# Optimization experiments

Hardware: AMD Instinct MI355X
Metric: run time of the kernel (lower is better)

The kernel has to match this reference:

```python
import jax, jax.numpy as jnp
import numpy as np

N, NOBJ, M, H, W = 512, 16, 8192, 128, 128


def _rand_rotations(key, n):
    A = jax.random.normal(key, (n, 3, 3), dtype=jnp.float32)
    q, r = jnp.linalg.qr(A)
    q = q * jnp.sign(jnp.diagonal(r, axis1=-2, axis2=-1))[:, None, :]
    det = jnp.linalg.det(q)  # +-1; flip first column if det == -1
    q = q.at[:, :, 0].multiply(det[:, None])
    return q


def setup_inputs() -> dict:
    key = jax.random.key(0)
    ks = jax.random.split(key, 10)
    obj_id = jax.random.randint(ks[0], (N,), 0, NOBJ, dtype=jnp.int32)
    # realistic pinhole intrinsics (pixels), slight per-sample jitter
    base_K = jnp.array([[600.0, 0.0, 64.0], [0.0, 600.0, 64.0], [0.0, 0.0, 1.0]], jnp.float32)
    cam_K = base_K[None] + jax.random.normal(ks[1], (N, 3, 3)) * jnp.array(
        [[5.0, 0.0, 1.0], [0.0, 5.0, 1.0], [0.0, 0.0, 0.0]], jnp.float32)
    gt_R = _rand_rotations(ks[2], N)
    # small rotational perturbation for pred
    pred_R = _rand_rotations(ks[3], N) @ gt_R
    gt_t = jnp.concatenate([jax.random.normal(ks[4], (N, 2)) * 20.0,
                            500.0 + jax.random.uniform(ks[4], (N, 1)) * 300.0], axis=-1)
    pred_t = gt_t + jax.random.normal(ks[5], (N, 3)) * 5.0
    mesh_points = jax.random.normal(ks[6], (NOBJ, M, 3)) * 50.0  # mm-scale meshes
    diameters = 150.0 + jax.random.uniform(ks[7], (NOBJ,)) * 150.0
    gt_coord_3d_roi = jax.random.normal(ks[8], (N, 3, H, W)) * 50.0
    gt_mask_vis_roi = jax.random.bernoulli(ks[9], 0.4, (N, 1, H, W))
    return dict(obj_id=obj_id, cam_K=cam_K, gt_cam_R_m2c=gt_R, gt_cam_t_m2c=gt_t,
                pred_cam_R_m2c=pred_R, pred_cam_t_m2c=pred_t,
                gt_coord_3d_roi=gt_coord_3d_roi, gt_mask_vis_roi=gt_mask_vis_roi,
                mesh_points=mesh_points, diameters=diameters)


def _project(K, x):
    # K: [N,3,3], x: [N,...,3] -> pixel coords [N,...,2]
    h = jnp.einsum('nij,n...j->n...i', K, x)
    return h[..., :2] / h[..., 2:3]


def reference(obj_id, cam_K, gt_cam_R_m2c, gt_cam_t_m2c, pred_cam_R_m2c,
              pred_cam_t_m2c, gt_coord_3d_roi, gt_mask_vis_roi, mesh_points, diameters):
    # RE (degrees)
    R_diff = pred_cam_R_m2c @ jnp.swapaxes(gt_cam_R_m2c, -2, -1)
    trace = R_diff[..., 0, 0] + R_diff[..., 1, 1] + R_diff[..., 2, 2]
    re = jnp.arccos((jnp.clip(trace, -1.0, 3.0) - 1.0) * 0.5) * (180.0 / jnp.pi)
    # TE (cm)
    te = jnp.linalg.norm(pred_cam_t_m2c - gt_cam_t_m2c, axis=-1) * 100.0
    # ADD: mean distance between transformed mesh points, / diameter
    pts = mesh_points[obj_id]                      # [N,M,3]
    dR = pred_cam_R_m2c - gt_cam_R_m2c
    dt = pred_cam_t_m2c - gt_cam_t_m2c
    diff = jnp.einsum('nij,nmj->nmi', dR, pts) + dt[:, None, :]
    ad = jnp.linalg.norm(diff, axis=-1).mean(axis=-1) / diameters[obj_id]
    # PROJ: mean projected distance over mesh points
    xp = jnp.einsum('nij,nmj->nmi', pred_cam_R_m2c, pts) + pred_cam_t_m2c[:, None, :]
    xg = jnp.einsum('nij,nmj->nmi', gt_cam_R_m2c, pts) + gt_cam_t_m2c[:, None, :]
    pj = jnp.linalg.norm(_project(cam_K, xp) - _project(cam_K, xg), axis=-1).mean(axis=-1)
    # PROJ-visible: same over visible ROI pixels (masked mean instead of ragged gather)
    verts = jnp.transpose(gt_coord_3d_roi, (0, 2, 3, 1))  # [N,H,W,3]
    vp = jnp.einsum('nij,nhwj->nhwi', pred_cam_R_m2c, verts) + pred_cam_t_m2c[:, None, None, :]
    vg = jnp.einsum('nij,nhwj->nhwi', gt_cam_R_m2c, verts) + gt_cam_t_m2c[:, None, None, :]
    d = jnp.linalg.norm(_project(cam_K, vp) - _project(cam_K, vg), axis=-1)  # [N,H,W]
    mask = gt_mask_vis_roi[:, 0].astype(d.dtype)
    pv = (d * mask).sum(axis=(1, 2)) / jnp.maximum(mask.sum(axis=(1, 2)), 1.0)
    return re, te, ad, pj, pv
```

## Files before the change

### kernel.cpp

```cpp
#include <hip/hip_runtime.h>
#include <math.h>

#define NS    512
#define NOBJ  16
#define MPTS  8192
#define HH    128
#define WW    128
#define HW    (HH * WW)
#define BLOCK 512
#define NWAVE (BLOCK / 64)
#define WSPAN (HW / NWAVE)
#define GRP   256
#define STG   2
#define NSTG  (WSPAN / (GRP * STG))
#define M_IT  (MPTS / 4 / BLOCK)

typedef float f4 __attribute__((ext_vector_type(4)));
typedef int   i4 __attribute__((ext_vector_type(4)));

__device__ __forceinline__ float frcp(float x)  { return __builtin_amdgcn_rcpf(x); }
__device__ __forceinline__ float fsqrt(float x) { return __builtin_amdgcn_sqrtf(x); }
__device__ __forceinline__ float rfl(float x) {
    return __int_as_float(__builtin_amdgcn_readfirstlane(__float_as_int(x)));
}
__device__ __forceinline__ void sched_fence() {
#if __has_builtin(__builtin_amdgcn_sched_barrier)
    __builtin_amdgcn_sched_barrier(0);
#endif
}
__device__ __forceinline__ f4 ntl_f4(const f4* p) {
#if __has_builtin(__builtin_nontemporal_load)
    return __builtin_nontemporal_load(p);
#else
    return *p;
#endif
}
__device__ __forceinline__ i4 ntl_i4(const i4* p) {
#if __has_builtin(__builtin_nontemporal_load)
    return __builtin_nontemporal_load(p);
#else
    return *p;
#endif
}

__device__ __forceinline__ void fuse_proj(const float* __restrict__ cam_K,
                                          const float* __restrict__ R,
                                          const float* __restrict__ t, int n,
                                          float A[9], float b[3]) {
    float K[9], Rr[9], tt[3];
#pragma unroll
    for (int i = 0; i < 9; ++i) { K[i] = cam_K[n * 9 + i]; Rr[i] = R[n * 9 + i]; }
#pragma unroll
    for (int i = 0; i < 3; ++i) tt[i] = t[n * 3 + i];
#pragma unroll
    for (int r = 0; r < 3; ++r) {
#pragma unroll
        for (int c = 0; c < 3; ++c)
            A[r * 3 + c] = rfl(K[r * 3 + 0] * Rr[0 * 3 + c]
                             + K[r * 3 + 1] * Rr[1 * 3 + c]
                             + K[r * 3 + 2] * Rr[2 * 3 + c]);
        b[r] = rfl(K[r * 3 + 0] * tt[0] + K[r * 3 + 1] * tt[1] + K[r * 3 + 2] * tt[2]);
    }
}

__global__ __attribute__((amdgpu_flat_work_group_size(BLOCK, BLOCK),
                          amdgpu_waves_per_eu(4, 4)))
void score_kernel(
    const int*   __restrict__ obj_id,
    const float* __restrict__ cam_K,
    const float* __restrict__ gt_R,
    const float* __restrict__ gt_t,
    const float* __restrict__ pr_R,
    const float* __restrict__ pr_t,
    const float* __restrict__ coord,
    const int*   __restrict__ mask,
    const float* __restrict__ mesh,
    const float* __restrict__ diam,
    float*       __restrict__ out)
{
    const int n    = blockIdx.x;
    const int tid  = threadIdx.x;
    const int w    = tid >> 6;
    const int lane = tid & 63;

    float Ap[9], Ag[9], bp[3], bg[3], dR[9], dt[3];
    fuse_proj(cam_K, pr_R, pr_t, n, Ap, bp);
    fuse_proj(cam_K, gt_R, gt_t, n, Ag, bg);
#pragma unroll
    for (int i = 0; i < 9; ++i) dR[i] = rfl(pr_R[n * 9 + i] - gt_R[n * 9 + i]);
#pragma unroll
    for (int i = 0; i < 3; ++i) dt[i] = rfl(pr_t[n * 3 + i] - gt_t[n * 3 + i]);
    const int obj = __builtin_amdgcn_readfirstlane(obj_id[n]);

    const float* cx = coord + (size_t)n * 3 * HW;
    const float* cy = cx + HW;
    const float* cz = cx + 2 * HW;
    const int*   mk = mask + (size_t)n * HW;
    const int wbase = w * WSPAN + 4 * lane;

    f4 X[2][STG], Y[2][STG], Z[2][STG];
    i4 Mq[2][STG];

#define LOAD_STAGE(s, b)                                                     \
    {                                                                        \
        _Pragma("unroll")                                                    \
        for (int g = 0; g < STG; ++g) {                                      \
            const int p = wbase + (s) * (STG * GRP) + g * GRP;               \
            X[b][g]  = ntl_f4((const f4*)(cx + p));                          \
            Y[b][g]  = ntl_f4((const f4*)(cy + p));                          \
            Z[b][g]  = ntl_f4((const f4*)(cz + p));                          \
            Mq[b][g] = ntl_i4((const i4*)(mk + p));                          \
        }                                                                    \
    }

    LOAD_STAGE(0, 0)
    LOAD_STAGE(1, 1)
    sched_fence();

    float s_pv = 0.0f, s_m = 0.0f;
#pragma unroll
    for (int s = 0; s < NSTG; ++s) {
        const int b = s & 1;
#pragma unroll
        for (int g = 0; g < STG; ++g) {
            const float xs[4] = {X[b][g].x, X[b][g].y, X[b][g].z, X[b][g].w};
            const float ys[4] = {Y[b][g].x, Y[b][g].y, Y[b][g].z, Y[b][g].w};
            const float zs[4] = {Z[b][g].x, Z[b][g].y, Z[b][g].z, Z[b][g].w};
            const int   ms[4] = {Mq[b][g].x, Mq[b][g].y, Mq[b][g].z, Mq[b][g].w};
#pragma unroll
            for (int j = 0; j < 4; ++j) {
                const float x = xs[j], y = ys[j], z = zs[j];
                const float hpx = fmaf(Ap[0], x, fmaf(Ap[1], y, fmaf(Ap[2], z, bp[0])));
                const float hpy = fmaf(Ap[3], x, fmaf(Ap[4], y, fmaf(Ap[5], z, bp[1])));
                const float hpz = fmaf(Ap[6], x, fmaf(Ap[7], y, fmaf(Ap[8], z, bp[2])));
                const float hgx = fmaf(Ag[0], x, fmaf(Ag[1], y, fmaf(Ag[2], z, bg[0])));
                const float hgy = fmaf(Ag[3], x, fmaf(Ag[4], y, fmaf(Ag[5], z, bg[1])));
                const float hgz = fmaf(Ag[6], x, fmaf(Ag[7], y, fmaf(Ag[8], z, bg[2])));
                const float iwp = frcp(hpz), iwg = frcp(hgz);
                const float du = fmaf(hpx, iwp, -hgx * iwg);
                const float dv = fmaf(hpy, iwp, -hgy * iwg);
                const float d  = fsqrt(fmaf(du, du, dv * dv));
                const float fm = (ms[j] != 0) ? 1.0f : 0.0f;
                s_pv += d * fm;
                s_m  += fm;
            }
        }
        if (s + 2 < NSTG) {
            LOAD_STAGE(s + 2, b)
            sched_fence();
        }
    }

    const f4* mp4 = (const f4*)(mesh + (size_t)obj * MPTS * 3);
    f4 MF[M_IT][3];
#pragma unroll
    for (int it = 0; it < M_IT; ++it) {
        const int k = it * BLOCK + tid;
        MF[it][0] = mp4[k * 3 + 0];
        MF[it][1] = mp4[k * 3 + 1];
        MF[it][2] = mp4[k * 3 + 2];
    }
    sched_fence();

    float s_ad = 0.0f, s_pj = 0.0f;
#pragma unroll
    for (int it = 0; it < M_IT; ++it) {
        const f4 f0 = MF[it][0], f1 = MF[it][1], f2 = MF[it][2];
        const float px[4] = {f0.x, f0.w, f1.z, f2.y};
        const float py[4] = {f0.y, f1.x, f1.w, f2.z};
        const float pz[4] = {f0.z, f1.y, f2.x, f2.w};
#pragma unroll
        for (int j = 0; j < 4; ++j) {
            const float x = px[j], y = py[j], z = pz[j];
            const float dx = fmaf(dR[0], x, fmaf(dR[1], y, fmaf(dR[2], z, dt[0])));
            const float dy = fmaf(dR[3], x, fmaf(dR[4], y, fmaf(dR[5], z, dt[1])));
            const float dz = fmaf(dR[6], x, fmaf(dR[7], y, fmaf(dR[8], z, dt[2])));
            s_ad += fsqrt(fmaf(dx, dx, fmaf(dy, dy, dz * dz)));
            const float hpx = fmaf(Ap[0], x, fmaf(Ap[1], y, fmaf(Ap[2], z, bp[0])));
            const float hpy = fmaf(Ap[3], x, fmaf(Ap[4], y, fmaf(Ap[5], z, bp[1])));
            const float hpz = fmaf(Ap[6], x, fmaf(Ap[7], y, fmaf(Ap[8], z, bp[2])));
            const float hgx = fmaf(Ag[0], x, fmaf(Ag[1], y, fmaf(Ag[2], z, bg[0])));
            const float hgy = fmaf(Ag[3], x, fmaf(Ag[4], y, fmaf(Ag[5], z, bg[1])));
            const float hgz = fmaf(Ag[6], x, fmaf(Ag[7], y, fmaf(Ag[8], z, bg[2])));
            const float iwp = frcp(hpz), iwg = frcp(hgz);
            const float du = fmaf(hpx, iwp, -hgx * iwg);
            const float dv = fmaf(hpy, iwp, -hgy * iwg);
            s_pj += fsqrt(fmaf(du, du, dv * dv));
        }
    }

    float vals[4] = {s_ad, s_pj, s_pv, s_m};
#pragma unroll
    for (int k = 0; k < 4; ++k)
#pragma unroll
        for (int off = 32; off > 0; off >>= 1)
            vals[k] += __shfl_down(vals[k], off, 64);

    __shared__ float red[4][NWAVE];
    if (lane == 0) {
#pragma unroll
        for (int k = 0; k < 4; ++k) red[k][w] = vals[k];
    }
    __syncthreads();

    if (tid == 0) {
        float tot[4];
#pragma unroll
        for (int k = 0; k < 4; ++k) {
            float s = 0.0f;
#pragma unroll
            for (int wv = 0; wv < NWAVE; ++wv) s += red[k][wv];
            tot[k] = s;
        }
        float Rg9[9], Rp9[9];
#pragma unroll
        for (int i = 0; i < 9; ++i) { Rg9[i] = gt_R[n * 9 + i]; Rp9[i] = pr_R[n * 9 + i]; }
        float trace = 0.0f;
#pragma unroll
        for (int i = 0; i < 9; ++i) trace += Rp9[i] * Rg9[i];
        trace = fminf(fmaxf(trace, -1.0f), 3.0f);
        const float te = sqrtf(dt[0] * dt[0] + dt[1] * dt[1] + dt[2] * dt[2]) * 100.0f;

        out[0 * NS + n] = acosf((trace - 1.0f) * 0.5f) * (180.0f / 3.14159265358979323846f);
        out[1 * NS + n] = te;
        out[2 * NS + n] = tot[0] * (1.0f / MPTS) / diam[obj];
        out[3 * NS + n] = tot[1] * (1.0f / MPTS);
        out[4 * NS + n] = tot[2] / fmaxf(tot[3], 1.0f);
    }
}

extern "C" void kernel_launch(void* const* d_in, const int* in_sizes, int n_in,
                              void* d_out, int out_size, void* d_ws, size_t ws_size,
                              hipStream_t stream) {
    const int*   obj_id = (const int*)  d_in[0];
    const float* cam_K  = (const float*)d_in[1];
    const float* gt_R   = (const float*)d_in[2];
    const float* gt_t   = (const float*)d_in[3];
    const float* pr_R   = (const float*)d_in[4];
    const float* pr_t   = (const float*)d_in[5];
    const float* coord  = (const float*)d_in[6];
    const int*   mask   = (const int*)  d_in[7];
    const float* mesh   = (const float*)d_in[8];
    const float* diam   = (const float*)d_in[9];
    float* out = (float*)d_out;

    score_kernel<<<NS, BLOCK, 0, stream>>>(obj_id, cam_K, gt_R, gt_t, pr_R, pr_t,
                                           coord, mask, mesh, diam, out);
}
```

Measured before the change: 182.8 us.

## Split fused scoring kernel into pixel-reduction and mesh/finalize kernels

Splits the single per-sample kernel into two launches. The first handles the visible-pixel projection reduction over 4 blocks per sample with 256-thread blocks and higher waves-per-EU, writing partial sums to workspace. The second computes the mesh ADD/PROJ sums and the final metrics, and combines the pixel partials. This aims to raise occupancy and parallelism on the memory-bound pixel stream. The cost is an extra launch, a workspace round trip, and removal of the explicit scheduling fences and mesh prefetch.

```diff
diff --git a/kernel.cpp b/kernel.cpp
--- a/kernel.cpp
+++ b/kernel.cpp
@@ -7,13 +7,15 @@
 #define HH    128
 #define WW    128
 #define HW    (HH * WW)
-#define BLOCK 512
-#define NWAVE (BLOCK / 64)
-#define WSPAN (HW / NWAVE)
-#define GRP   256
-#define STG   2
-#define NSTG  (WSPAN / (GRP * STG))
-#define M_IT  (MPTS / 4 / BLOCK)
+
+#define PXB   256
+#define QS    4
+#define PXW   (HW / QS / 4)
+#define PSTG  256
+#define PNST  (PXW / PSTG)
+
+#define FXB   256
+#define M_IT  (MPTS / 4 / FXB)
 
 typedef float f4 __attribute__((ext_vector_type(4)));
 typedef int   i4 __attribute__((ext_vector_type(4)));
@@ -22,11 +24,6 @@
 __device__ __forceinline__ float fsqrt(float x) { return __builtin_amdgcn_sqrtf(x); }
 __device__ __forceinline__ float rfl(float x) {
     return __int_as_float(__builtin_amdgcn_readfirstlane(__float_as_int(x)));
-}
-__device__ __forceinline__ void sched_fence() {
-#if __has_builtin(__builtin_amdgcn_sched_barrier)
-    __builtin_amdgcn_sched_barrier(0);
-#endif
 }
 __device__ __forceinline__ f4 ntl_f4(const f4* p) {
 #if __has_builtin(__builtin_nontemporal_load)
@@ -63,10 +60,9 @@
     }
 }
 
-__global__ __attribute__((amdgpu_flat_work_group_size(BLOCK, BLOCK),
-                          amdgpu_waves_per_eu(4, 4)))
-void score_kernel(
-    const int*   __restrict__ obj_id,
+__global__ __attribute__((amdgpu_flat_work_group_size(PXB, PXB),
+                          amdgpu_waves_per_eu(8, 8)))
+void pixel_kernel(
     const float* __restrict__ cam_K,
     const float* __restrict__ gt_R,
     const float* __restrict__ gt_t,
@@ -74,8 +70,96 @@
     const float* __restrict__ pr_t,
     const float* __restrict__ coord,
     const int*   __restrict__ mask,
+    float*       __restrict__ ws)
+{
+    const int bid  = blockIdx.x;
+    const int n    = bid >> 2;
+    const int q    = bid & (QS - 1);
+    const int tid  = threadIdx.x;
+    const int w    = tid >> 6;
+    const int lane = tid & 63;
+
+    float Ap[9], Ag[9], bp[3], bg[3];
+    fuse_proj(cam_K, pr_R, pr_t, n, Ap, bp);
+    fuse_proj(cam_K, gt_R, gt_t, n, Ag, bg);
+
+    const int base = q * (HW / QS) + w * PXW + 4 * lane;
+    const float* cx = coord + (size_t)n * 3 * HW + base;
+    const float* cy = cx + HW;
+    const float* cz = cx + 2 * HW;
+    const int*   mk = mask + (size_t)n * HW + base;
+
+    f4 X[2], Y[2], Z[2];
+    i4 Mq[2];
+
+#define PLOAD(s, b)                                                          \
+    {                                                                        \
+        const int p = (s) * PSTG;                                            \
+        X[b]  = ntl_f4((const f4*)(cx + p));                                 \
+        Y[b]  = ntl_f4((const f4*)(cy + p));                                 \
+        Z[b]  = ntl_f4((const f4*)(cz + p));                                 \
+        Mq[b] = ntl_i4((const i4*)(mk + p));                                 \
+    }
+
+    PLOAD(0, 0)
+    PLOAD(1, 1)
+
+    float s_pv = 0.0f, s_m = 0.0f;
+#pragma unroll
+    for (int s = 0; s < PNST; ++s) {
+        const int b = s & 1;
+        const float xs[4] = {X[b].x, X[b].y, X[b].z, X[b].w};
+        const float ys[4] = {Y[b].x, Y[b].y, Y[b].z, Y[b].w};
+        const float zs[4] = {Z[b].x, Z[b].y, Z[b].z, Z[b].w};
+        const int   ms[4] = {Mq[b].x, Mq[b].y, Mq[b].z, Mq[b].w};
+#pragma unroll
+        for (int j = 0; j < 4; ++j) {
+            const float x = xs[j], y = ys[j], z = zs[j];
+            const float hpx = fmaf(Ap[0], x, fmaf(Ap[1], y, fmaf(Ap[2], z, bp[0])));
+            const float hpy = fmaf(Ap[3], x, fmaf(Ap[4], y, fmaf(Ap[5], z, bp[1])));
+            const float hpz = fmaf(Ap[6], x, fmaf(Ap[7], y, fmaf(Ap[8], z, bp[2])));
+            const float hgx = fmaf(Ag[0], x, fmaf(Ag[1], y, fmaf(Ag[2], z, bg[0])));
+            const float hgy = fmaf(Ag[3], x, fmaf(Ag[4], y, fmaf(Ag[5], z, bg[1])));
+            const float hgz = fmaf(Ag[6], x, fmaf(Ag[7], y, fmaf(Ag[8], z, bg[2])));
+            const float iwp = frcp(hpz), iwg = frcp(hgz);
+            const float du = fmaf(hpx, iwp, -hgx * iwg);
+            const float dv = fmaf(hpy, iwp, -hgy * iwg);
+            const float d  = fsqrt(fmaf(du, du, dv * dv));
+            const float fm = (ms[j] != 0) ? 1.0f : 0.0f;
+            s_pv += d * fm;
+            s_m  += fm;
+        }
+        if (s + 2 < PNST) PLOAD(s + 2, b)
+    }
+
+#pragma unroll
+    for (int off = 32; off > 0; off >>= 1) {
+        s_pv += __shfl_down(s_pv, off, 64);
+        s_m  += __shfl_down(s_m,  off, 64);
+    }
+    __shared__ float red[2][PXB / 64];
+    if (lane == 0) { red[0][w] = s_pv; red[1][w] = s_m; }
+    __syncthreads();
+    if (tid == 0) {
+        float a = 0.0f, m = 0.0f;
+#pragma unroll
+        for (int wv = 0; wv < PXB / 64; ++wv) { a += red[0][wv]; m += red[1][wv]; }
+        ws[bid * 2 + 0] = a;
+        ws[bid * 2 + 1] = m;
+    }
+}
+
+__global__ __launch_bounds__(FXB)
+void final_kernel(
+    const int*   __restrict__ obj_id,
+    const float* __restrict__ cam_K,
+    const float* __restrict__ gt_R,
+    const float* __restrict__ gt_t,
+    const float* __restrict__ pr_R,
+    const float* __restrict__ pr_t,
     const float* __restrict__ mesh,
     const float* __restrict__ diam,
+    const float* __restrict__ ws,
     float*       __restrict__ out)
 {
     const int n    = blockIdx.x;
@@ -92,80 +176,15 @@
     for (int i = 0; i < 3; ++i) dt[i] = rfl(pr_t[n * 3 + i] - gt_t[n * 3 + i]);
     const int obj = __builtin_amdgcn_readfirstlane(obj_id[n]);
 
-    const float* cx = coord + (size_t)n * 3 * HW;
-    const float* cy = cx + HW;
-    const float* cz = cx + 2 * HW;
-    const int*   mk = mask + (size_t)n * HW;
-    const int wbase = w * WSPAN + 4 * lane;
-
-    f4 X[2][STG], Y[2][STG], Z[2][STG];
-    i4 Mq[2][STG];
-
-#define LOAD_STAGE(s, b)                                                     \
-    {                                                                        \
-        _Pragma("unroll")                                                    \
-        for (int g = 0; g < STG; ++g) {                                      \
-            const int p = wbase + (s) * (STG * GRP) + g * GRP;               \
-            X[b][g]  = ntl_f4((const f4*)(cx + p));                          \
-            Y[b][g]  = ntl_f4((const f4*)(cy + p));                          \
-            Z[b][g]  = ntl_f4((const f4*)(cz + p));                          \
-            Mq[b][g] = ntl_i4((const i4*)(mk + p));                          \
-        }                                                                    \
-    }
-
-    LOAD_STAGE(0, 0)
-    LOAD_STAGE(1, 1)
-    sched_fence();
-
-    float s_pv = 0.0f, s_m = 0.0f;
-#pragma unroll
-    for (int s = 0; s < NSTG; ++s) {
-        const int b = s & 1;
-#pragma unroll
-        for (int g = 0; g < STG; ++g) {
-            const float xs[4] = {X[b][g].x, X[b][g].y, X[b][g].z, X[b][g].w};
-            const float ys[4] = {Y[b][g].x, Y[b][g].y, Y[b][g].z, Y[b][g].w};
-            const float zs[4] = {Z[b][g].x, Z[b][g].y, Z[b][g].z, Z[b][g].w};
-            const int   ms[4] = {Mq[b][g].x, Mq[b][g].y, Mq[b][g].z, Mq[b][g].w};
-#pragma unroll
-            for (int j = 0; j < 4; ++j) {
-                const float x = xs[j], y = ys[j], z = zs[j];
-                const float hpx = fmaf(Ap[0], x, fmaf(Ap[1], y, fmaf(Ap[2], z, bp[0])));
-                const float hpy = fmaf(Ap[3], x, fmaf(Ap[4], y, fmaf(Ap[5], z, bp[1])));
-                const float hpz = fmaf(Ap[6], x, fmaf(Ap[7], y, fmaf(Ap[8], z, bp[2])));
-                const float hgx = fmaf(Ag[0], x, fmaf(Ag[1], y, fmaf(Ag[2], z, bg[0])));
-                const float hgy = fmaf(Ag[3], x, fmaf(Ag[4], y, fmaf(Ag[5], z, bg[1])));
-                const float hgz = fmaf(Ag[6], x, fmaf(Ag[7], y, fmaf(Ag[8], z, bg[2])));
-                const float iwp = frcp(hpz), iwg = frcp(hgz);
-                const float du = fmaf(hpx, iwp, -hgx * iwg);
-                const float dv = fmaf(hpy, iwp, -hgy * iwg);
-                const float d  = fsqrt(fmaf(du, du, dv * dv));
-                const float fm = (ms[j] != 0) ? 1.0f : 0.0f;
-                s_pv += d * fm;
-                s_m  += fm;
-            }
-        }
-        if (s + 2 < NSTG) {
-            LOAD_STAGE(s + 2, b)
-            sched_fence();
-        }
-    }
-
     const f4* mp4 = (const f4*)(mesh + (size_t)obj * MPTS * 3);
-    f4 MF[M_IT][3];
+
+    float s_ad = 0.0f, s_pj = 0.0f;
 #pragma unroll
     for (int it = 0; it < M_IT; ++it) {
-        const int k = it * BLOCK + tid;
-        MF[it][0] = mp4[k * 3 + 0];
-        MF[it][1] = mp4[k * 3 + 1];
-        MF[it][2] = mp4[k * 3 + 2];
-    }
-    sched_fence();
-
-    float s_ad = 0.0f, s_pj = 0.0f;
-#pragma unroll
-    for (int it = 0; it < M_IT; ++it) {
-        const f4 f0 = MF[it][0], f1 = MF[it][1], f2 = MF[it][2];
+        const int k = it * FXB + tid;
+        const f4 f0 = mp4[k * 3 + 0];
+        const f4 f1 = mp4[k * 3 + 1];
+        const f4 f2 = mp4[k * 3 + 2];
         const float px[4] = {f0.x, f0.w, f1.z, f2.y};
         const float py[4] = {f0.y, f1.x, f1.w, f2.z};
         const float pz[4] = {f0.z, f1.y, f2.x, f2.w};
@@ -189,29 +208,27 @@
         }
     }
 
-    float vals[4] = {s_ad, s_pj, s_pv, s_m};
-#pragma unroll
-    for (int k = 0; k < 4; ++k)
-#pragma unroll
-        for (int off = 32; off > 0; off >>= 1)
-            vals[k] += __shfl_down(vals[k], off, 64);
-
-    __shared__ float red[4][NWAVE];
-    if (lane == 0) {
-#pragma unroll
-        for (int k = 0; k < 4; ++k) red[k][w] = vals[k];
-    }
+#pragma unroll
+    for (int off = 32; off > 0; off >>= 1) {
+        s_ad += __shfl_down(s_ad, off, 64);
+        s_pj += __shfl_down(s_pj, off, 64);
+    }
+    __shared__ float red[2][FXB / 64];
+    if (lane == 0) { red[0][w] = s_ad; red[1][w] = s_pj; }
     __syncthreads();
 
     if (tid == 0) {
-        float tot[4];
-#pragma unroll
-        for (int k = 0; k < 4; ++k) {
-            float s = 0.0f;
-#pragma unroll
-            for (int wv = 0; wv < NWAVE; ++wv) s += red[k][wv];
-            tot[k] = s;
+        float ad = 0.0f, pj = 0.0f;
+#pragma unroll
+        for (int wv = 0; wv < FXB / 64; ++wv) { ad += red[0][wv]; pj += red[1][wv]; }
+
+        float pv_d = 0.0f, pv_m = 0.0f;
+#pragma unroll
+        for (int qq = 0; qq < QS; ++qq) {
+            pv_d += ws[(n * QS + qq) * 2 + 0];
+            pv_m += ws[(n * QS + qq) * 2 + 1];
         }
+
         float Rg9[9], Rp9[9];
 #pragma unroll
         for (int i = 0; i < 9; ++i) { Rg9[i] = gt_R[n * 9 + i]; Rp9[i] = pr_R[n * 9 + i]; }
@@ -223,9 +240,9 @@
 
         out[0 * NS + n] = acosf((trace - 1.0f) * 0.5f) * (180.0f / 3.14159265358979323846f);
         out[1 * NS + n] = te;
-        out[2 * NS + n] = tot[0] * (1.0f / MPTS) / diam[obj];
-        out[3 * NS + n] = tot[1] * (1.0f / MPTS);
-        out[4 * NS + n] = tot[2] / fmaxf(tot[3], 1.0f);
+        out[2 * NS + n] = ad * (1.0f / MPTS) / diam[obj];
+        out[3 * NS + n] = pj * (1.0f / MPTS);
+        out[4 * NS + n] = pv_d / fmaxf(pv_m, 1.0f);
     }
 }
 
@@ -243,7 +260,10 @@
     const float* mesh   = (const float*)d_in[8];
     const float* diam   = (const float*)d_in[9];
     float* out = (float*)d_out;
-
-    score_kernel<<<NS, BLOCK, 0, stream>>>(obj_id, cam_K, gt_R, gt_t, pr_R, pr_t,
-                                           coord, mask, mesh, diam, out);
-}
+    float* ws  = (float*)d_ws;
+
+    pixel_kernel<<<NS * QS, PXB, 0, stream>>>(cam_K, gt_R, gt_t, pr_R, pr_t,
+                                              coord, mask, ws);
+    final_kernel<<<NS, FXB, 0, stream>>>(obj_id, cam_K, gt_R, gt_t, pr_R, pr_t,
+                                         mesh, diam, ws, out);
+}
```

New measurement: 187.4 us. +2.5%, slower.
